# Performance work log

Measured on AMD Instinct MI355X. Metric: run time of the kernel, lower is better.

Reference implementation:

```python
import jax, jax.numpy as jnp
import numpy as np

B, T, C, H = 128, 256, 384, 6
D = C // H  # head dim = 64


def setup_inputs() -> dict:
    key = jax.random.key(0)
    k1, k2, k3, k4, k5 = jax.random.split(key, 5)
    s = 0.02
    return {
        "x": jax.random.normal(k1, (B, T, C), dtype=jnp.float32),
        "W_qkv": jax.random.normal(k2, (C, 3 * C), dtype=jnp.float32) * s,
        "b_qkv": jax.random.normal(k3, (3 * C,), dtype=jnp.float32) * s,
        "W_proj": jax.random.normal(k4, (C, C), dtype=jnp.float32) * s,
        "b_proj": jax.random.normal(k5, (C,), dtype=jnp.float32) * s,
    }


def reference(x, W_qkv, b_qkv, W_proj, b_proj):
    Bv, Tv, Cv = x.shape
    # fused QKV projection, then split
    qkv = x @ W_qkv + b_qkv                      # [B,T,3C]
    q, k, v = jnp.split(qkv, 3, axis=-1)
    # [B,T,C] -> [B,H,T,D]
    q = q.reshape(Bv, Tv, H, D).transpose(0, 2, 1, 3)
    k = k.reshape(Bv, Tv, H, D).transpose(0, 2, 1, 3)
    v = v.reshape(Bv, Tv, H, D).transpose(0, 2, 1, 3)
    # causal masked scores, scaled by head_dim**-0.5
    scores = jnp.einsum("bhqd,bhkd->bhqk", q, k) * (D ** -0.5)
    causal = jnp.tril(jnp.ones((Tv, Tv), dtype=bool))
    scores = jnp.where(causal, scores, -jnp.inf)
    wt = jax.nn.softmax(scores, axis=-1)
    # dropout layers are identity in eval mode
    out = jnp.einsum("bhqk,bhkd->bhqd", wt, v)   # [B,H,T,D]
    out = out.transpose(0, 2, 1, 3).reshape(Bv, Tv, Cv)
    return out @ W_proj + b_proj
```

## Files before the change

kernel.cpp:

```cpp
#include <hip/hip_runtime.h>

typedef unsigned short u16;
typedef unsigned int u32;
typedef __attribute__((ext_vector_type(4))) float f32x4;
typedef __attribute__((ext_vector_type(8))) __bf16 bf16x8;
typedef __attribute__((ext_vector_type(2))) __bf16 bf16x2;

#define NEGINF (-1e30f)
#define QSCALE 0.18033688011112042f

__device__ __forceinline__ u16 f32_to_bf16(float f) {
  union { float f; unsigned int u; } v;
  v.f = f;
  unsigned int u = v.u;
  u += 0x7fffu + ((u >> 16) & 1u);
  return (u16)(u >> 16);
}

__device__ __forceinline__ u32 pk_bf16(float a, float b) {
  bf16x2 t;
  t.x = (__bf16)a;
  t.y = (__bf16)b;
  return __builtin_bit_cast(u32, t);
}

__device__ __forceinline__ f32x4 mfma_bf16(bf16x8 a, bf16x8 b, f32x4 c) {
  return __builtin_amdgcn_mfma_f32_16x16x32_bf16(a, b, c, 0, 0, 0);
}

#define GLOAD_LDS16(g, l) __builtin_amdgcn_global_load_lds( \
    (const __attribute__((address_space(1))) unsigned int*)(g), \
    (__attribute__((address_space(3))) unsigned int*)(l), 16, 0, 0)

__global__ void k_cvt4(const float4* __restrict__ in, u16* __restrict__ out, int nq) {
  int i = blockIdx.x * blockDim.x + threadIdx.x;
  if (i >= nq) return;
  float4 v = in[i];
  uint2 o;
  o.x = (unsigned int)f32_to_bf16(v.x) | ((unsigned int)f32_to_bf16(v.y) << 16);
  o.y = (unsigned int)f32_to_bf16(v.z) | ((unsigned int)f32_to_bf16(v.w) << 16);
  *(uint2*)(out + (size_t)i * 4) = o;
}

__global__ void k_tcvt(const float* __restrict__ in, u16* __restrict__ out, int K, int N) {
  int idx = blockIdx.x * blockDim.x + threadIdx.x;
  if (idx >= K * N) return;
  int k = idx / N, n = idx - k * N;
  out[(size_t)n * K + k] = f32_to_bf16(in[idx]);
}

__device__ __forceinline__ void gemm256x64(
    const u16* __restrict__ A, const u16* __restrict__ Bt,
    int mBase, int nBase, u16* lsA, u16* lsB,
    f32x4 acc[4][2], int lane, int wv, int wm, int wn) {
  const int l15 = lane & 15;
  size_t aoff[4];
  u32 aldso[4];
#pragma unroll
  for (int jj = 0; jj < 4; ++jj) {
    int c = wv * 256 + jj * 64 + lane;
    int row = c >> 3;
    int kc = (c & 7) ^ (row & 7);
    aoff[jj] = (size_t)(mBase + row) * 384 + kc * 8;
    aldso[jj] = (u32)(wv * 256 + jj * 64) * 8;
  }
  int cb = wv * 64 + lane;
  int brow = cb >> 3;
  size_t boff = (size_t)(nBase + brow) * 384 + (size_t)(((cb & 7) ^ (brow & 7)) * 8);
  u32 bldso = (u32)(wv * 64) * 8;

#define STAGE_T(kt, buf) do { \
  _Pragma("unroll") \
  for (int jj = 0; jj < 4; ++jj) \
    GLOAD_LDS16(A + aoff[jj] + (kt), lsA + (buf) * 16384 + aldso[jj]); \
  GLOAD_LDS16(Bt + boff + (kt), lsB + (buf) * 4096 + bldso); \
  } while (0)

  STAGE_T(0, 0);
#pragma unroll
  for (int t = 0; t < 6; ++t) {
    const int cur = t & 1;
    if (t < 5) {
      STAGE_T((t + 1) * 64, cur ^ 1);
      asm volatile("s_waitcnt vmcnt(5)" ::: "memory");
    } else {
      asm volatile("s_waitcnt vmcnt(0)" ::: "memory");
    }
    __builtin_amdgcn_s_barrier();
    const char* bA = (const char*)(lsA + cur * 16384);
    const char* bB = (const char*)(lsB + cur * 4096);
#pragma unroll
    for (int ks = 0; ks < 2; ++ks) {
      bf16x8 af[4], bfr[2];
#pragma unroll
      for (int i = 0; i < 4; ++i) {
        int row = wm * 64 + i * 16 + l15;
        af[i] = *(const bf16x8*)(bA + row * 128 + (((ks * 4 + (lane >> 4)) ^ (row & 7)) << 4));
      }
#pragma unroll
      for (int j = 0; j < 2; ++j) {
        int row = wn * 32 + j * 16 + l15;
        bfr[j] = *(const bf16x8*)(bB + row * 128 + (((ks * 4 + (lane >> 4)) ^ (row & 7)) << 4));
      }
#pragma unroll
      for (int i = 0; i < 4; ++i)
#pragma unroll
        for (int j = 0; j < 2; ++j)
          acc[i][j] = mfma_bf16(af[i], bfr[j], acc[i][j]);
    }
    __builtin_amdgcn_s_barrier();
  }
#undef STAGE_T
}

__global__ __launch_bounds__(512, 4) void k_qkv(
    const u16* __restrict__ A, const u16* __restrict__ Bt,
    const float* __restrict__ bias,
    u16* __restrict__ Qb, u16* __restrict__ Kb, u16* __restrict__ Vtb) {
  __shared__ __align__(16) u16 lsA[2 * 16384];
  __shared__ __align__(16) u16 lsB[2 * 4096];
  const int tid = threadIdx.x, lane = tid & 63, wv = tid >> 6;
  const int l15 = lane & 15, g = lane >> 4;
  const int wm = wv >> 1, wn = wv & 1;
  const int bid = (int)blockIdx.x;
  const int wgid = (bid & 7) * 288 + (bid >> 3);
  const int mtile = wgid / 18, ntile = wgid % 18;
  const int mBase = mtile * 256, nBase = ntile * 64;
  f32x4 acc[4][2] = {};
  gemm256x64(A, Bt, mBase, nBase, lsA, lsB, acc, lane, wv, wm, wn);

  const int part = nBase / 384;
  const int cbase = nBase - part * 384;
#pragma unroll
  for (int j = 0; j < 2; ++j) {
    int c = cbase + wn * 32 + j * 16 + l15;
    float bv = bias[nBase + wn * 32 + j * 16 + l15];
    int hh = c >> 6, d = c & 63;
    size_t bhh = (size_t)(mtile * 6 + hh);
#pragma unroll
    for (int i = 0; i < 4; ++i) {
      int t0 = wm * 64 + i * 16 + g * 4;
      if (part == 2) {
        uint2 w;
        w.x = pk_bf16(acc[i][j][0] + bv, acc[i][j][1] + bv);
        w.y = pk_bf16(acc[i][j][2] + bv, acc[i][j][3] + bv);
        *(uint2*)(Vtb + (bhh * 64 + d) * 256 + t0) = w;
      } else if (part == 0) {
#pragma unroll
        for (int r = 0; r < 4; ++r)
          Qb[(bhh * 256 + t0 + r) * 64 + d] = f32_to_bf16((acc[i][j][r] + bv) * QSCALE);
      } else {
#pragma unroll
        for (int r = 0; r < 4; ++r)
          Kb[(bhh * 256 + t0 + r) * 64 + d] = f32_to_bf16(acc[i][j][r] + bv);
      }
    }
  }
}

__global__ __launch_bounds__(64, 2) void k_attn(
    const u16* __restrict__ Qb, const u16* __restrict__ Kb,
    const u16* __restrict__ Vtb, u16* __restrict__ Ob) {
  __shared__ __align__(16) u16 lsP[64 * 64];
  const int lane = threadIdx.x;
  const int l15 = lane & 15, g = lane >> 4;
  const int qt = 3 - (int)blockIdx.y;
  const int bh = blockIdx.x;
  const int b = bh / 6, h = bh % 6;
  const u16* Qh = Qb + (size_t)bh * (256 * 64);
  const u16* Kh = Kb + (size_t)bh * (256 * 64);
  const u16* Vh = Vtb + (size_t)bh * (64 * 256);

  bf16x8 qf[2][4];
#pragma unroll
  for (int ks = 0; ks < 2; ++ks)
#pragma unroll
    for (int iq = 0; iq < 4; ++iq)
      qf[ks][iq] = *(const bf16x8*)(Qh + (size_t)(qt * 64 + iq * 16 + l15) * 64 + ks * 32 + g * 8);

  f32x4 o[4][4] = {};
  float rl[4] = {0.f, 0.f, 0.f, 0.f};

  bf16x8 kf[2][4], vf[2][4];
#pragma unroll
  for (int ks = 0; ks < 2; ++ks)
#pragma unroll
    for (int jk = 0; jk < 4; ++jk)
      kf[ks][jk] = *(const bf16x8*)(Kh + (size_t)(jk * 16 + l15) * 64 + ks * 32 + g * 8);

  for (int kt = 0; kt <= qt; ++kt) {
    f32x4 st[4][4] = {};
#pragma unroll
    for (int ks = 0; ks < 2; ++ks)
#pragma unroll
      for (int jk = 0; jk < 4; ++jk)
#pragma unroll
        for (int iq = 0; iq < 4; ++iq)
          st[jk][iq] = mfma_bf16(kf[ks][jk], qf[ks][iq], st[jk][iq]);

#pragma unroll
    for (int ks = 0; ks < 2; ++ks)
#pragma unroll
      for (int jd = 0; jd < 4; ++jd)
        vf[ks][jd] = *(const bf16x8*)(Vh + (size_t)(jd * 16 + l15) * 256 + kt * 64 + ks * 32 + g * 8);
    if (kt < qt) {
#pragma unroll
      for (int ks = 0; ks < 2; ++ks)
#pragma unroll
        for (int jk = 0; jk < 4; ++jk)
          kf[ks][jk] = *(const bf16x8*)(Kh + (size_t)((kt + 1) * 64 + jk * 16 + l15) * 64 + ks * 32 + g * 8);
    }

    if (kt == qt) {
#pragma unroll
      for (int jk = 0; jk < 4; ++jk)
#pragma unroll
        for (int iq = 0; iq < 4; ++iq)
#pragma unroll
          for (int r = 0; r < 4; ++r)
            if (jk * 16 + g * 4 + r > iq * 16 + l15) st[jk][iq][r] = NEGINF;
    }

    float rs[4] = {0.f, 0.f, 0.f, 0.f};
#pragma unroll
    for (int jk = 0; jk < 4; ++jk)
#pragma unroll
      for (int iq = 0; iq < 4; ++iq) {
        float p0 = __builtin_amdgcn_exp2f(st[jk][iq][0]);
        float p1 = __builtin_amdgcn_exp2f(st[jk][iq][1]);
        float p2 = __builtin_amdgcn_exp2f(st[jk][iq][2]);
        float p3 = __builtin_amdgcn_exp2f(st[jk][iq][3]);
        rs[iq] += (p0 + p1) + (p2 + p3);
        int qrow = iq * 16 + l15;
        int byte = (qrow * 128 + (jk * 16 + g * 4) * 2) ^ ((qrow & 7) << 4);
        uint2 w;
        w.x = pk_bf16(p0, p1);
        w.y = pk_bf16(p2, p3);
        *(uint2*)((char*)lsP + byte) = w;
      }
#pragma unroll
    for (int iq = 0; iq < 4; ++iq) {
      float v = rs[iq];
      v += __shfl_xor(v, 16);
      v += __shfl_xor(v, 32);
      rl[iq] += v;
    }

#pragma unroll
    for (int ks = 0; ks < 2; ++ks) {
      bf16x8 pf[4];
#pragma unroll
      for (int iq = 0; iq < 4; ++iq) {
        int qrow = iq * 16 + l15;
        pf[iq] = *(const bf16x8*)((char*)lsP + ((qrow * 128 + ks * 64 + g * 16) ^ ((qrow & 7) << 4)));
      }
#pragma unroll
      for (int jd = 0; jd < 4; ++jd)
#pragma unroll
        for (int iq = 0; iq < 4; ++iq)
          o[jd][iq] = mfma_bf16(vf[ks][jd], pf[iq], o[jd][iq]);
    }
  }

#pragma unroll
  for (int iq = 0; iq < 4; ++iq) {
    float inv = 1.0f / rl[iq];
    int t = qt * 64 + iq * 16 + l15;
#pragma unroll
    for (int jd = 0; jd < 4; ++jd) {
      uint2 w;
      w.x = pk_bf16(o[jd][iq][0] * inv, o[jd][iq][1] * inv);
      w.y = pk_bf16(o[jd][iq][2] * inv, o[jd][iq][3] * inv);
      *(uint2*)(Ob + ((size_t)(b * 256 + t)) * 384 + h * 64 + jd * 16 + g * 4) = w;
    }
  }
}

__global__ __launch_bounds__(512, 4) void k_proj(
    const u16* __restrict__ A, const u16* __restrict__ Bt,
    const float* __restrict__ bias, float* __restrict__ out) {
  __shared__ __align__(16) u16 lsA[2 * 16384];
  __shared__ __align__(16) u16 lsB[2 * 4096];
  const int tid = threadIdx.x, lane = tid & 63, wv = tid >> 6;
  const int l15 = lane & 15, g = lane >> 4;
  const int wm = wv >> 1, wn = wv & 1;
  const int bid = (int)blockIdx.x;
  const int wgid = (bid & 7) * 96 + (bid >> 3);
  const int mtile = wgid / 6, ntile = wgid % 6;
  const int mBase = mtile * 256, nBase = ntile * 64;
  f32x4 acc[4][2] = {};
  gemm256x64(A, Bt, mBase, nBase, lsA, lsB, acc, lane, wv, wm, wn);
#pragma unroll
  for (int j = 0; j < 2; ++j) {
    int col = nBase + wn * 32 + j * 16 + l15;
    float bv = bias[col];
#pragma unroll
    for (int i = 0; i < 4; ++i) {
      int m0 = mBase + wm * 64 + i * 16 + g * 4;
#pragma unroll
      for (int r = 0; r < 4; ++r)
        out[(size_t)(m0 + r) * 384 + col] = acc[i][j][r] + bv;
    }
  }
}

extern "C" void kernel_launch(void* const* d_in, const int* in_sizes, int n_in,
                              void* d_out, int out_size, void* d_ws, size_t ws_size,
                              hipStream_t stream) {
  const float* x     = (const float*)d_in[0];
  const float* Wqkv  = (const float*)d_in[1];
  const float* bqkv  = (const float*)d_in[2];
  const float* Wproj = (const float*)d_in[3];
  const float* bproj = (const float*)d_in[4];
  float* out = (float*)d_out;

  char* ws = (char*)d_ws;
  u16* xb     = (u16*)(ws);
  u16* wqkvb  = (u16*)(ws + 25165824);
  u16* wprojb = (u16*)(ws + 26050560);
  u16* Qb     = (u16*)(ws + 26345472);
  u16* Kb     = (u16*)(ws + 51511296);
  u16* Vtb    = (u16*)(ws + 76677120);
  u16* Ob     = (u16*)(ws + 101842944);

  k_cvt4<<<12288, 256, 0, stream>>>((const float4*)x, xb, 3145728);
  k_tcvt<<<1728, 256, 0, stream>>>(Wqkv, wqkvb, 384, 1152);
  k_tcvt<<<576, 256, 0, stream>>>(Wproj, wprojb, 384, 384);
  k_qkv<<<2304, 512, 0, stream>>>(xb, wqkvb, bqkv, Qb, Kb, Vtb);
  k_attn<<<dim3(768, 4), 64, 0, stream>>>(Qb, Kb, Vtb, Ob);
  k_proj<<<768, 512, 0, stream>>>(Ob, wprojb, bproj, out);
}
```

Before: 138.0 us.

## Merge four query-tile attention wavefronts into one 256-thread block with staged output stores

The attention kernel now launches one 256-thread block per batch-head, with each of the four wavefronts handling one query tile, instead of a grid of single-wave blocks. Each wave gets its own LDS buffer for P, and the output is staged through that LDS buffer so it can be written as coalesced 16-byte row stores instead of scattered 8-byte stores. s_setprio is raised around the MFMA bursts and the kt loop is kept rolled. Causal work is uneven across the waves (wave 3 does four times the work of wave 0), so a block stays resident until its longest wave finishes.

Result: slower. 216.5 us (+56.9%).

```diff
diff --git a/kernel.cpp b/kernel.cpp
--- a/kernel.cpp
+++ b/kernel.cpp
@@ -158,18 +158,19 @@
   }
 }
 
-__global__ __launch_bounds__(64, 2) void k_attn(
+__global__ __launch_bounds__(256, 4) void k_attn(
     const u16* __restrict__ Qb, const u16* __restrict__ Kb,
     const u16* __restrict__ Vtb, u16* __restrict__ Ob) {
-  __shared__ __align__(16) u16 lsP[64 * 64];
-  const int lane = threadIdx.x;
+  __shared__ __align__(16) u16 lsP[4][64 * 64];
+  const int lane = threadIdx.x & 63, wv = threadIdx.x >> 6;
   const int l15 = lane & 15, g = lane >> 4;
-  const int qt = 3 - (int)blockIdx.y;
+  const int qt = wv;
   const int bh = blockIdx.x;
   const int b = bh / 6, h = bh % 6;
   const u16* Qh = Qb + (size_t)bh * (256 * 64);
   const u16* Kh = Kb + (size_t)bh * (256 * 64);
   const u16* Vh = Vtb + (size_t)bh * (64 * 256);
+  char* pbuf = (char*)&lsP[wv][0];
 
   bf16x8 qf[2][4];
 #pragma unroll
@@ -188,8 +189,10 @@
     for (int jk = 0; jk < 4; ++jk)
       kf[ks][jk] = *(const bf16x8*)(Kh + (size_t)(jk * 16 + l15) * 64 + ks * 32 + g * 8);
 
+#pragma unroll 1
   for (int kt = 0; kt <= qt; ++kt) {
     f32x4 st[4][4] = {};
+    __builtin_amdgcn_s_setprio(1);
 #pragma unroll
     for (int ks = 0; ks < 2; ++ks)
 #pragma unroll
@@ -197,6 +200,7 @@
 #pragma unroll
         for (int iq = 0; iq < 4; ++iq)
           st[jk][iq] = mfma_bf16(kf[ks][jk], qf[ks][iq], st[jk][iq]);
+    __builtin_amdgcn_s_setprio(0);
 
 #pragma unroll
     for (int ks = 0; ks < 2; ++ks)
@@ -236,7 +240,7 @@
         uint2 w;
         w.x = pk_bf16(p0, p1);
         w.y = pk_bf16(p2, p3);
-        *(uint2*)((char*)lsP + byte) = w;
+        *(uint2*)(pbuf + byte) = w;
       }
 #pragma unroll
     for (int iq = 0; iq < 4; ++iq) {
@@ -252,27 +256,39 @@
 #pragma unroll
       for (int iq = 0; iq < 4; ++iq) {
         int qrow = iq * 16 + l15;
-        pf[iq] = *(const bf16x8*)((char*)lsP + ((qrow * 128 + ks * 64 + g * 16) ^ ((qrow & 7) << 4)));
-      }
+        pf[iq] = *(const bf16x8*)(pbuf + ((qrow * 128 + ks * 64 + g * 16) ^ ((qrow & 7) << 4)));
+      }
+      __builtin_amdgcn_s_setprio(1);
 #pragma unroll
       for (int jd = 0; jd < 4; ++jd)
 #pragma unroll
         for (int iq = 0; iq < 4; ++iq)
           o[jd][iq] = mfma_bf16(vf[ks][jd], pf[iq], o[jd][iq]);
+      __builtin_amdgcn_s_setprio(0);
     }
   }
 
 #pragma unroll
   for (int iq = 0; iq < 4; ++iq) {
     float inv = 1.0f / rl[iq];
-    int t = qt * 64 + iq * 16 + l15;
+    int row = iq * 16 + l15;
 #pragma unroll
     for (int jd = 0; jd < 4; ++jd) {
       uint2 w;
       w.x = pk_bf16(o[jd][iq][0] * inv, o[jd][iq][1] * inv);
       w.y = pk_bf16(o[jd][iq][2] * inv, o[jd][iq][3] * inv);
-      *(uint2*)(Ob + ((size_t)(b * 256 + t)) * 384 + h * 64 + jd * 16 + g * 4) = w;
-    }
+      int byte = (row * 128 + jd * 32 + g * 8) ^ ((row & 7) << 4);
+      *(uint2*)(pbuf + byte) = w;
+    }
+  }
+  asm volatile("s_waitcnt lgkmcnt(0)" ::: "memory");
+#pragma unroll
+  for (int rep = 0; rep < 8; ++rep) {
+    int row = rep * 8 + (lane >> 3);
+    int c = lane & 7;
+    uint4 v = *(const uint4*)(pbuf + row * 128 + ((c ^ (row & 7)) * 16));
+    int t = qt * 64 + row;
+    *(uint4*)(Ob + ((size_t)(b * 256 + t)) * 384 + h * 64 + c * 8) = v;
   }
 }
 
@@ -327,6 +343,6 @@
   k_tcvt<<<1728, 256, 0, stream>>>(Wqkv, wqkvb, 384, 1152);
   k_tcvt<<<576, 256, 0, stream>>>(Wproj, wprojb, 384, 384);
   k_qkv<<<2304, 512, 0, stream>>>(xb, wqkvb, bqkv, Qb, Kb, Vtb);
-  k_attn<<<dim3(768, 4), 64, 0, stream>>>(Qb, Kb, Vtb, Ob);
+  k_attn<<<768, 256, 0, stream>>>(Qb, Kb, Vtb, Ob);
   k_proj<<<768, 512, 0, stream>>>(Ob, wprojb, bproj, out);
 }
```
